# Kernel tuning notes

Measured on AMD Instinct MI355X. Metric: run time of the kernel, lower is better.

## Reference

```python
import jax, jax.numpy as jnp
import numpy as np
import math

M = 0.5
S = 64.0
TH = math.cos(math.pi - M)           # threshold cos(pi - m)
MM = math.sin(math.pi - M) * M       # sin(pi - m) * m
EPS = 1e-12

def _l2norm(x, axis=-1):
    return x / jnp.sqrt(jnp.sum(x * x, axis=axis, keepdims=True) + EPS)

def setup_inputs() -> dict:
    key = jax.random.key(0)
    k1, k2, k3 = jax.random.split(key, 3)
    B, D, C = 512, 512, 100000
    features = jax.random.normal(k1, (B, D), dtype=jnp.float32)
    weight = jax.random.normal(k2, (C, D), dtype=jnp.float32)
    labels = jax.random.randint(k3, (B,), 0, C, dtype=jnp.int32)
    return {"features": features, "labels": labels, "weight": weight}

def reference(features, labels, weight):
    # cos_theta: [B, C] = normalized features @ normalized weight^T
    cos_theta = jnp.einsum('bd,cd->bc', _l2norm(features), _l2norm(weight))
    cos_theta = jnp.clip(cos_theta, -1.0, 1.0)
    B = features.shape[0]
    rows = jnp.arange(B)
    # margin correction only affects the target column per row; gather it
    tgt_cos = cos_theta[rows, labels]                      # [B]
    theta_m = jnp.arccos(tgt_cos) + M
    cos_theta_m = jnp.cos(theta_m)
    tgt_adj = jnp.where(tgt_cos > TH, cos_theta_m, tgt_cos - MM)
    output = cos_theta.at[rows, labels].set(tgt_adj)
    return S * output
```

## Files before the change

### kernel.cpp

```cpp
#include <hip/hip_runtime.h>


typedef __attribute__((ext_vector_type(8))) short short8;
typedef __attribute__((ext_vector_type(8))) unsigned short u16x8;
typedef __attribute__((ext_vector_type(4))) float f32x4;

#define TH_CONST  (-0.8775825618903728f)
#define MM_CONST  (0.23971276930210156f)
#define M_MARGIN  0.5f
#define S_SCALE   64.0f
#define KD 512

__device__ __forceinline__ unsigned short f2bf(float x) {
    unsigned int u = __float_as_uint(x);
    u += 0x7fffu + ((u >> 16) & 1u);
    return (unsigned short)(u >> 16);
}

__global__ __launch_bounds__(256)
void convert_norm_kernel(const float* __restrict__ W,
                         const float* __restrict__ F,
                         unsigned short* __restrict__ Wb,
                         unsigned short* __restrict__ Fb,
                         float* __restrict__ invW,
                         float* __restrict__ invF,
                         const int C, const int B)
{
    const int lane = threadIdx.x & 63;
    const int half = lane >> 5;
    const int l5   = lane & 31;
    const int total  = C + B;
    const int npairs = (total + 1) >> 1;

    int pair = blockIdx.x * 4 + (threadIdx.x >> 6);
    const int stride = gridDim.x * 4;

    for (; pair < npairs; pair += stride) {
        const int row = pair * 2 + half;
        const bool valid = (row < total);
        float ss = 0.f;
        float* inv = nullptr;
        unsigned short* dst = nullptr;

        if (valid) {
            const float* src;
            if (row < C) {
                src = W + (size_t)row * KD;
                dst = Wb + (size_t)row * KD;
                inv = invW + row;
            } else {
                const int r = row - C;
                src = F + (size_t)r * KD;
                dst = Fb + (size_t)r * KD;
                inv = invF + r;
            }
            const float4* p = (const float4*)(src + l5 * 16);
            float4 v0 = p[0], v1 = p[1], v2 = p[2], v3 = p[3];

            ss = v0.x*v0.x + v0.y*v0.y + v0.z*v0.z + v0.w*v0.w
               + v1.x*v1.x + v1.y*v1.y + v1.z*v1.z + v1.w*v1.w
               + v2.x*v2.x + v2.y*v2.y + v2.z*v2.z + v2.w*v2.w
               + v3.x*v3.x + v3.y*v3.y + v3.z*v3.z + v3.w*v3.w;

            u16x8 pk0, pk1;
            pk0[0]=f2bf(v0.x); pk0[1]=f2bf(v0.y); pk0[2]=f2bf(v0.z); pk0[3]=f2bf(v0.w);
            pk0[4]=f2bf(v1.x); pk0[5]=f2bf(v1.y); pk0[6]=f2bf(v1.z); pk0[7]=f2bf(v1.w);
            pk1[0]=f2bf(v2.x); pk1[1]=f2bf(v2.y); pk1[2]=f2bf(v2.z); pk1[3]=f2bf(v2.w);
            pk1[4]=f2bf(v3.x); pk1[5]=f2bf(v3.y); pk1[6]=f2bf(v3.z); pk1[7]=f2bf(v3.w);
            *(u16x8*)(dst + l5 * 16)     = pk0;
            *(u16x8*)(dst + l5 * 16 + 8) = pk1;
        }

        ss += __shfl_xor(ss, 1);
        ss += __shfl_xor(ss, 2);
        ss += __shfl_xor(ss, 4);
        ss += __shfl_xor(ss, 8);
        ss += __shfl_xor(ss, 16);
        if (valid && l5 == 0) *inv = 1.0f / sqrtf(ss + 1e-12f);
    }
}

__device__ __forceinline__ void gload_lds_16(const void* g, void* l) {
    __builtin_amdgcn_global_load_lds(
        (const __attribute__((address_space(1))) unsigned int*)g,
        (__attribute__((address_space(3))) unsigned int*)l,
        16, 0, 0);
}

__global__ __launch_bounds__(256, 4)
void arcface_gemm_kernel(const unsigned short* __restrict__ Fb,
                         const unsigned short* __restrict__ Wb,
                         const float* __restrict__ invF,
                         const float* __restrict__ invW,
                         const int*   __restrict__ labels,
                         float*       __restrict__ Out,
                         const int C, const int GM)
{
    __shared__ unsigned short As[128 * 64];
    __shared__ unsigned short Bs[128 * 64];
    __shared__ float nF[128];
    __shared__ float nW[128];
    __shared__ int   Ls[128];

    const int nwg = gridDim.x;
    const int bid = blockIdx.x;
    const int q   = nwg >> 3, rr = nwg & 7;
    const int xcd = bid & 7,  seq = bid >> 3;
    const int wg  = (xcd < rr ? xcd * (q + 1) : rr * (q + 1) + (xcd - rr) * q) + seq;
    const int mt  = wg % GM;
    const int nt  = wg / GM;

    const int m_base = mt * 128;
    const int n_base = nt * 128;

    const int t    = threadIdx.x;
    const int wave = t >> 6;
    const int lane = t & 63;
    const int wm   = (wave >> 1) * 64;
    const int wn   = (wave & 1) * 64;
    const int quad = lane >> 4;
    const int lcol = lane & 15;

    if (t < 128) {
        nF[t] = invF[m_base + t];
        const int c = n_base + t;
        nW[t] = (c < C) ? invW[c] : 0.f;
        Ls[t] = labels[m_base + t];
    }

    const int rbase  = t >> 3;
    const int colSwz = (((t & 7) ^ ((t >> 3) & 7)) << 4);

    const char* gA = (const char*)Fb + (size_t)(m_base + rbase) * (KD * 2) + colSwz;

    unsigned int offB[4];
    #pragma unroll
    for (int c = 0; c < 4; ++c) {
        int rb = n_base + c * 32 + rbase;
        if (rb >= C) rb = C - 1;
        offB[c] = (unsigned int)rb * (KD * 2) + colSwz;
    }
    const char* gWb = (const char*)Wb;

    char* lA = (char*)As + wave * 1024;
    char* lB = (char*)Bs + wave * 1024;

    f32x4 acc[4][4];
    #pragma unroll
    for (int i = 0; i < 4; ++i)
        #pragma unroll
        for (int j = 0; j < 4; ++j)
            acc[i][j] = (f32x4){0.f, 0.f, 0.f, 0.f};

    const int sw = (lcol & 7) << 4;

    #pragma unroll 1
    for (int kt = 0; kt < KD / 64; ++kt) {
        const int ko = kt * 128;
        #pragma unroll
        for (int c = 0; c < 4; ++c)
            gload_lds_16(gA + c * 32768 + ko, lA + c * 4096);
        #pragma unroll
        for (int c = 0; c < 4; ++c)
            gload_lds_16(gWb + offB[c] + ko, lB + c * 4096);
        __syncthreads();

        short8 af[4], bfr[4];
        #pragma unroll
        for (int i = 0; i < 4; ++i) {
            const int ra = (wm + i * 16 + lcol) * 128;
            const int rb = (wn + i * 16 + lcol) * 128;
            const int co = (quad * 16) ^ sw;
            af[i]  = *(const short8*)((const char*)As + ra + co);
            bfr[i] = *(const short8*)((const char*)Bs + rb + co);
        }
        #pragma unroll
        for (int i = 0; i < 4; ++i)
            #pragma unroll
            for (int j = 0; j < 4; ++j)
                acc[i][j] = __builtin_amdgcn_mfma_f32_16x16x32_bf16(
                                af[i], bfr[j], acc[i][j], 0, 0, 0);
        #pragma unroll
        for (int i = 0; i < 4; ++i) {
            const int ra = (wm + i * 16 + lcol) * 128;
            const int rb = (wn + i * 16 + lcol) * 128;
            const int co = (64 | (quad * 16)) ^ sw;
            af[i]  = *(const short8*)((const char*)As + ra + co);
            bfr[i] = *(const short8*)((const char*)Bs + rb + co);
        }
        #pragma unroll
        for (int i = 0; i < 4; ++i)
            #pragma unroll
            for (int j = 0; j < 4; ++j)
                acc[i][j] = __builtin_amdgcn_mfma_f32_16x16x32_bf16(
                                af[i], bfr[j], acc[i][j], 0, 0, 0);
        __syncthreads();
    }

    #pragma unroll
    for (int mi = 0; mi < 4; ++mi) {
        const int rl_base = wm + mi * 16 + quad * 4;
        #pragma unroll
        for (int rg = 0; rg < 4; ++rg) {
            const int rl = rl_base + rg;
            const float invf = nF[rl];
            const int lbl = Ls[rl];
            float* orow = Out + (size_t)(m_base + rl) * C;
            #pragma unroll
            for (int ni = 0; ni < 4; ++ni) {
                const int cl = wn + ni * 16 + lcol;
                const int gcol = n_base + cl;
                if (gcol < C) {
                    float v = acc[mi][ni][rg] * invf * nW[cl];
                    v = fminf(1.0f, fmaxf(-1.0f, v));
                    if (gcol == lbl) {
                        v = (v > TH_CONST) ? cosf(acosf(v) + M_MARGIN)
                                           : (v - MM_CONST);
                    }
                    __builtin_nontemporal_store(S_SCALE * v, &orow[gcol]);
                }
            }
        }
    }
}

#define BM 128
#define BN 128
#define BK 32

__global__ __launch_bounds__(256, 2)
void arcface_fused_kernel(const float* __restrict__ F,
                          const int*   __restrict__ labels,
                          const float* __restrict__ W,
                          float*       __restrict__ Out,
                          const int C)
{
    __shared__ unsigned short Asf[BM][BK];
    __shared__ unsigned short Bsf[BN][BK];
    __shared__ float normF[BM];
    __shared__ float normW[BN];
    __shared__ int   Lsf[BM];

    const int t = threadIdx.x;
    const int m_base = blockIdx.x * BM;
    const int n_base = blockIdx.y * BN;

    if (t < BM) Lsf[t] = labels[m_base + t];

    const int r = t >> 1;
    const int h = t & 1;

    const int lane = t & 63;
    const int wave = t >> 6;
    const int wm = (wave >> 1) * 64;
    const int wn = (wave & 1) * 64;
    const int quad = lane >> 4;
    const int lcol = lane & 15;

    f32x4 acc[4][4];
    #pragma unroll
    for (int i = 0; i < 4; ++i)
        #pragma unroll
        for (int j = 0; j < 4; ++j)
            acc[i][j] = (f32x4){0.f, 0.f, 0.f, 0.f};

    const int cls = n_base + r;
    const bool cvalid = (cls < C);

    const float* Arow = F + (size_t)(m_base + r) * KD + h * 16;
    const float* Wrow = W + (size_t)(cvalid ? cls : 0) * KD + h * 16;

    float sF = 0.f, sW = 0.f;

    for (int kt = 0; kt < KD / BK; ++kt) {
        const float4* ap = (const float4*)(Arow + kt * BK);
        const float4* wp = (const float4*)(Wrow + kt * BK);
        float4 a0 = ap[0], a1 = ap[1], a2 = ap[2], a3 = ap[3];
        float4 w0, w1, w2, w3;
        if (cvalid) { w0 = wp[0]; w1 = wp[1]; w2 = wp[2]; w3 = wp[3]; }
        else { w0 = make_float4(0.f,0.f,0.f,0.f); w1 = w0; w2 = w0; w3 = w0; }

        sF += a0.x*a0.x + a0.y*a0.y + a0.z*a0.z + a0.w*a0.w
            + a1.x*a1.x + a1.y*a1.y + a1.z*a1.z + a1.w*a1.w
            + a2.x*a2.x + a2.y*a2.y + a2.z*a2.z + a2.w*a2.w
            + a3.x*a3.x + a3.y*a3.y + a3.z*a3.z + a3.w*a3.w;
        sW += w0.x*w0.x + w0.y*w0.y + w0.z*w0.z + w0.w*w0.w
            + w1.x*w1.x + w1.y*w1.y + w1.z*w1.z + w1.w*w1.w
            + w2.x*w2.x + w2.y*w2.y + w2.z*w2.z + w2.w*w2.w
            + w3.x*w3.x + w3.y*w3.y + w3.z*w3.z + w3.w*w3.w;

        u16x8 pa0, pa1, pb0, pb1;
        pa0[0]=f2bf(a0.x); pa0[1]=f2bf(a0.y); pa0[2]=f2bf(a0.z); pa0[3]=f2bf(a0.w);
        pa0[4]=f2bf(a1.x); pa0[5]=f2bf(a1.y); pa0[6]=f2bf(a1.z); pa0[7]=f2bf(a1.w);
        pa1[0]=f2bf(a2.x); pa1[1]=f2bf(a2.y); pa1[2]=f2bf(a2.z); pa1[3]=f2bf(a2.w);
        pa1[4]=f2bf(a3.x); pa1[5]=f2bf(a3.y); pa1[6]=f2bf(a3.z); pa1[7]=f2bf(a3.w);
        pb0[0]=f2bf(w0.x); pb0[1]=f2bf(w0.y); pb0[2]=f2bf(w0.z); pb0[3]=f2bf(w0.w);
        pb0[4]=f2bf(w1.x); pb0[5]=f2bf(w1.y); pb0[6]=f2bf(w1.z); pb0[7]=f2bf(w1.w);
        pb1[0]=f2bf(w2.x); pb1[1]=f2bf(w2.y); pb1[2]=f2bf(w2.z); pb1[3]=f2bf(w2.w);
        pb1[4]=f2bf(w3.x); pb1[5]=f2bf(w3.y); pb1[6]=f2bf(w3.z); pb1[7]=f2bf(w3.w);

        __syncthreads();
        *((u16x8*)&Asf[r][h*16])     = pa0;
        *((u16x8*)&Asf[r][h*16 + 8]) = pa1;
        *((u16x8*)&Bsf[r][h*16])     = pb0;
        *((u16x8*)&Bsf[r][h*16 + 8]) = pb1;
        __syncthreads();

        short8 af[4], bfr[4];
        #pragma unroll
        for (int i = 0; i < 4; ++i) {
            af[i]  = *(const short8*)&Asf[wm + i*16 + lcol][quad*8];
            bfr[i] = *(const short8*)&Bsf[wn + i*16 + lcol][quad*8];
        }
        #pragma unroll
        for (int i = 0; i < 4; ++i)
            #pragma unroll
            for (int j = 0; j < 4; ++j)
                acc[i][j] = __builtin_amdgcn_mfma_f32_16x16x32_bf16(
                                af[i], bfr[j], acc[i][j], 0, 0, 0);
    }

    sF += __shfl_xor(sF, 1);
    sW += __shfl_xor(sW, 1);
    if (h == 0) {
        normF[r] = 1.0f / sqrtf(sF + 1e-12f);
        normW[r] = 1.0f / sqrtf(sW + 1e-12f);
    }
    __syncthreads();

    #pragma unroll
    for (int mi = 0; mi < 4; ++mi) {
        const int rl_base = wm + mi*16 + quad*4;
        #pragma unroll
        for (int rg = 0; rg < 4; ++rg) {
            const int rl = rl_base + rg;
            const float invf = normF[rl];
            const int lbl = Lsf[rl];
            float* orow = Out + (size_t)(m_base + rl) * C;
            #pragma unroll
            for (int ni = 0; ni < 4; ++ni) {
                const int cl = wn + ni*16 + lcol;
                const int gcol = n_base + cl;
                if (gcol < C) {
                    float v = acc[mi][ni][rg] * invf * normW[cl];
                    v = fminf(1.0f, fmaxf(-1.0f, v));
                    if (gcol == lbl) {
                        v = (v > TH_CONST) ? cosf(acosf(v) + M_MARGIN)
                                           : (v - MM_CONST);
                    }
                    orow[gcol] = S_SCALE * v;
                }
            }
        }
    }
}

extern "C" void kernel_launch(void* const* d_in, const int* in_sizes, int n_in,
                              void* d_out, int out_size, void* d_ws, size_t ws_size,
                              hipStream_t stream) {
    const float* F      = (const float*)d_in[0];
    const int*   labels = (const int*)d_in[1];
    const float* W      = (const float*)d_in[2];
    float*       Out    = (float*)d_out;

    const int B = in_sizes[1];
    const int C = in_sizes[2] / KD;

    const size_t a = 255;
    size_t offWb = 0;
    size_t szWb  = (size_t)C * KD * sizeof(unsigned short);
    size_t offFb = (offWb + szWb + a) & ~a;
    size_t szFb  = (size_t)B * KD * sizeof(unsigned short);
    size_t offIW = (offFb + szFb + a) & ~a;
    size_t szIW  = (size_t)C * sizeof(float);
    size_t offIF = (offIW + szIW + a) & ~a;
    size_t szIF  = (size_t)B * sizeof(float);
    size_t need  = offIF + szIF;

    if (d_ws != nullptr && ws_size >= need && (B % 128) == 0) {
        unsigned short* Wb   = (unsigned short*)((char*)d_ws + offWb);
        unsigned short* Fb   = (unsigned short*)((char*)d_ws + offFb);
        float*          invW = (float*)((char*)d_ws + offIW);
        float*          invF = (float*)((char*)d_ws + offIF);

        convert_norm_kernel<<<2048, 256, 0, stream>>>(W, F, Wb, Fb, invW, invF, C, B);

        const int GM = B / 128;
        const int NT = (C + 127) / 128;
        arcface_gemm_kernel<<<GM * NT, 256, 0, stream>>>(Fb, Wb, invF, invW,
                                                         labels, Out, C, GM);
    } else {
        dim3 grid(B / BM, (C + BN - 1) / BN);
        arcface_fused_kernel<<<grid, dim3(256), 0, stream>>>(F, labels, W, Out, C);
    }
}
```

Baseline: 448.8 us.

## Double-buffer LDS tiles in GEMM kernel to overlap global loads with MFMA

The GEMM main loop now uses two LDS buffers for the A and B tiles. The next k-tile is prefetched with global_load_lds while MFMAs run on the current one, and each iteration ends with a single waitcnt plus barrier. The occupancy hint drops from 4 to 2 workgroups per CU because LDS use doubles. The output store becomes a regular store instead of a nontemporal one, and the fallback grid rounds B up.

```diff
diff --git a/kernel.cpp b/kernel.cpp
--- a/kernel.cpp
+++ b/kernel.cpp
@@ -87,7 +87,7 @@
         16, 0, 0);
 }
 
-__global__ __launch_bounds__(256, 4)
+__global__ __launch_bounds__(256, 2)
 void arcface_gemm_kernel(const unsigned short* __restrict__ Fb,
                          const unsigned short* __restrict__ Wb,
                          const float* __restrict__ invF,
@@ -96,8 +96,8 @@
                          float*       __restrict__ Out,
                          const int C, const int GM)
 {
-    __shared__ unsigned short As[128 * 64];
-    __shared__ unsigned short Bs[128 * 64];
+    __shared__ unsigned short As[2][128 * 64];
+    __shared__ unsigned short Bs[2][128 * 64];
     __shared__ float nF[128];
     __shared__ float nW[128];
     __shared__ int   Ls[128];
@@ -154,47 +154,51 @@
 
     const int sw = (lcol & 7) << 4;
 
+    auto stage = [&](int kt, int nb) {
+        const int ko = kt * 128;
+        const int bo = nb * 16384;
+        #pragma unroll
+        for (int c = 0; c < 4; ++c)
+            gload_lds_16(gA + c * 32768 + ko, lA + bo + c * 4096);
+        #pragma unroll
+        for (int c = 0; c < 4; ++c)
+            gload_lds_16(gWb + offB[c] + ko, lB + bo + c * 4096);
+    };
+
+    auto compute = [&](int nb) {
+        const char* ab = (const char*)As + nb * 16384;
+        const char* bb = (const char*)Bs + nb * 16384;
+        #pragma unroll
+        for (int h = 0; h < 2; ++h) {
+            const int co = ((h * 64) | (quad * 16)) ^ sw;
+            short8 af[4], bfr[4];
+            #pragma unroll
+            for (int i = 0; i < 4; ++i) {
+                af[i]  = *(const short8*)(ab + (wm + i * 16 + lcol) * 128 + co);
+                bfr[i] = *(const short8*)(bb + (wn + i * 16 + lcol) * 128 + co);
+            }
+            #pragma unroll
+            for (int i = 0; i < 4; ++i)
+                #pragma unroll
+                for (int j = 0; j < 4; ++j)
+                    acc[i][j] = __builtin_amdgcn_mfma_f32_16x16x32_bf16(
+                                    af[i], bfr[j], acc[i][j], 0, 0, 0);
+        }
+    };
+
+    stage(0, 0);
+    asm volatile("s_waitcnt vmcnt(0)" ::: "memory");
+    __builtin_amdgcn_s_barrier();
+
     #pragma unroll 1
     for (int kt = 0; kt < KD / 64; ++kt) {
-        const int ko = kt * 128;
-        #pragma unroll
-        for (int c = 0; c < 4; ++c)
-            gload_lds_16(gA + c * 32768 + ko, lA + c * 4096);
-        #pragma unroll
-        for (int c = 0; c < 4; ++c)
-            gload_lds_16(gWb + offB[c] + ko, lB + c * 4096);
-        __syncthreads();
-
-        short8 af[4], bfr[4];
-        #pragma unroll
-        for (int i = 0; i < 4; ++i) {
-            const int ra = (wm + i * 16 + lcol) * 128;
-            const int rb = (wn + i * 16 + lcol) * 128;
-            const int co = (quad * 16) ^ sw;
-            af[i]  = *(const short8*)((const char*)As + ra + co);
-            bfr[i] = *(const short8*)((const char*)Bs + rb + co);
-        }
-        #pragma unroll
-        for (int i = 0; i < 4; ++i)
-            #pragma unroll
-            for (int j = 0; j < 4; ++j)
-                acc[i][j] = __builtin_amdgcn_mfma_f32_16x16x32_bf16(
-                                af[i], bfr[j], acc[i][j], 0, 0, 0);
-        #pragma unroll
-        for (int i = 0; i < 4; ++i) {
-            const int ra = (wm + i * 16 + lcol) * 128;
-            const int rb = (wn + i * 16 + lcol) * 128;
-            const int co = (64 | (quad * 16)) ^ sw;
-            af[i]  = *(const short8*)((const char*)As + ra + co);
-            bfr[i] = *(const short8*)((const char*)Bs + rb + co);
-        }
-        #pragma unroll
-        for (int i = 0; i < 4; ++i)
-            #pragma unroll
-            for (int j = 0; j < 4; ++j)
-                acc[i][j] = __builtin_amdgcn_mfma_f32_16x16x32_bf16(
-                                af[i], bfr[j], acc[i][j], 0, 0, 0);
-        __syncthreads();
+        const int cur = kt & 1;
+        if (kt < KD / 64 - 1)
+            stage(kt + 1, cur ^ 1);
+        __builtin_amdgcn_sched_barrier(0);
+        compute(cur);
+        asm volatile("s_waitcnt vmcnt(0)" ::: "memory");
+        __builtin_amdgcn_s_barrier();
     }
 
     #pragma unroll
@@ -217,7 +221,7 @@
                         v = (v > TH_CONST) ? cosf(acosf(v) + M_MARGIN)
                                            : (v - MM_CONST);
                     }
-                    __builtin_nontemporal_store(S_SCALE * v, &orow[gcol]);
+                    orow[gcol] = S_SCALE * v;
                 }
             }
         }
@@ -390,7 +394,7 @@
         arcface_gemm_kernel<<<GM * NT, 256, 0, stream>>>(Fb, Wb, invF, invW,
                                                          labels, Out, C, GM);
     } else {
-        dim3 grid(B / BM, (C + BN - 1) / BN);
+        dim3 grid((B + BM - 1) / BM, (C + BN - 1) / BN);
         arcface_fused_kernel<<<grid, dim3(256), 0, stream>>>(F, labels, W, Out, C);
     }
 }
```

After: 506.3 us. 12.8% more time.
